# Kernel optimization log

Hardware: AMD Instinct MI355X
Metric: run time of the kernel (lower is better)

## Reference

```python
import jax, jax.numpy as jnp
import numpy as np

B, L, D_MODEL, H = 4, 2048, 1024, 16
HD = D_MODEL // H  # head_dim = 64


def _rope_tables(seq_len, dim, dtype):
    inv_freq = 1.0 / (10000.0 ** (jnp.arange(0, dim, 2, dtype=jnp.float32) / dim))
    t = jnp.arange(seq_len, dtype=jnp.float32)
    freqs = jnp.outer(t, inv_freq)  # (S, dim/2)
    return jnp.cos(freqs).astype(dtype), jnp.sin(freqs).astype(dtype)


def _apply_rope(x):
    # x: (B, H, S, d)
    cos, sin = _rope_tables(x.shape[-2], x.shape[-1], x.dtype)  # (S, d/2)
    x_even = x[..., 0::2]
    x_odd = x[..., 1::2]
    out_even = x_even * cos - x_odd * sin
    out_odd = x_even * sin + x_odd * cos
    return jnp.stack([out_even, out_odd], axis=-1).reshape(x.shape)


def setup_inputs() -> dict:
    key = jax.random.key(0)
    ks = jax.random.split(key, 9)
    s = 1.0 / np.sqrt(D_MODEL)
    inp = {
        "query": jax.random.normal(ks[0], (B, L, D_MODEL), dtype=jnp.float32),
        "Wq": jax.random.uniform(ks[1], (D_MODEL, D_MODEL), jnp.float32, -s, s),
        "bq": jax.random.uniform(ks[2], (D_MODEL,), jnp.float32, -s, s),
        "Wk": jax.random.uniform(ks[3], (D_MODEL, D_MODEL), jnp.float32, -s, s),
        "bk": jax.random.uniform(ks[4], (D_MODEL,), jnp.float32, -s, s),
        "Wv": jax.random.uniform(ks[5], (D_MODEL, D_MODEL), jnp.float32, -s, s),
        "bv": jax.random.uniform(ks[6], (D_MODEL,), jnp.float32, -s, s),
        "Wo": jax.random.uniform(ks[7], (D_MODEL, D_MODEL), jnp.float32, -s, s),
        "bo": jax.random.uniform(ks[8], (D_MODEL,), jnp.float32, -s, s),
    }
    return inp


def reference(query, Wq, bq, Wk, bk, Wv, bv, Wo, bo):
    Bq, Lq, _ = query.shape
    # projections (torch Linear: x @ W.T + b), split into heads -> (B, H, L, d)
    def proj(x, W, b):
        y = x @ W.T + b
        return y.reshape(Bq, Lq, H, HD).transpose(0, 2, 1, 3)
    q = _apply_rope(proj(query, Wq, bq))
    k = _apply_rope(proj(query, Wk, bk))
    v = proj(query, Wv, bv)
    scores = jnp.einsum("bhqd,bhkd->bhqk", q, k) / np.sqrt(HD)
    causal_mask = jnp.triu(jnp.ones((Lq, Lq), dtype=bool), k=1)
    scores = jnp.where(causal_mask[None, None, :, :], -jnp.inf, scores)
    attn = jax.nn.softmax(scores, axis=-1)
    out = jnp.einsum("bhqk,bhkd->bhqd", attn, v)
    out = out.transpose(0, 2, 1, 3).reshape(Bq, Lq, D_MODEL)
    return out @ Wo.T + bo
```

## Files before the change

kernel.cpp:

```cpp
#include <hip/hip_runtime.h>
#include <hip/hip_bf16.h>
#include <math.h>

#define L_SEQ  2048
#define DMODEL 1024
#define NHEAD  16
#define HEADD  64

typedef __attribute__((ext_vector_type(8))) short short8;
typedef __attribute__((ext_vector_type(4))) short short4v;
typedef __attribute__((ext_vector_type(4))) float f32x4;

static __device__ __forceinline__ unsigned short f2bf(float f) {
    unsigned int u = __float_as_uint(f);
    unsigned int r = (u + 0x7fffu + ((u >> 16) & 1u)) >> 16;
    return (unsigned short)r;
}

static __device__ __forceinline__ void dma16(const unsigned short* g, unsigned short* l) {
    __builtin_amdgcn_global_load_lds((const __attribute__((address_space(1))) void*)g,
                                     (__attribute__((address_space(3))) void*)l, 16, 0, 0);
}

__global__ __launch_bounds__(256) void prep(
    const float* __restrict__ query,
    const float* __restrict__ Wq, const float* __restrict__ Wk,
    const float* __restrict__ Wv, const float* __restrict__ Wo,
    unsigned short* __restrict__ xb, unsigned short* __restrict__ wdst,
    float* __restrict__ rope)
{
    int gid = blockIdx.x * 256 + threadIdx.x;
    if (gid < 2097152) {
        float4 v = reinterpret_cast<const float4*>(query)[gid];
        ushort4 o;
        o.x = f2bf(v.x); o.y = f2bf(v.y); o.z = f2bf(v.z); o.w = f2bf(v.w);
        reinterpret_cast<ushort4*>(xb)[gid] = o;
    } else if (gid < 2097152 + 1048576) {
        int i = gid - 2097152;
        int which = i >> 18;
        const float* src = which == 0 ? Wq : which == 1 ? Wk : which == 2 ? Wv : Wo;
        float4 v = reinterpret_cast<const float4*>(src)[i & 262143];
        ushort4 o;
        o.x = f2bf(v.x); o.y = f2bf(v.y); o.z = f2bf(v.z); o.w = f2bf(v.w);
        reinterpret_cast<ushort4*>(wdst)[i] = o;
    } else if (gid < 2097152 + 1048576 + 65536) {
        int i = gid - (2097152 + 1048576);
        int lpos = i >> 5, i2 = i & 31;
        float inv_f = expf(-0.28782313662425574f * (float)i2);
        float ang = (float)lpos * inv_f;
        rope[2 * i]     = cosf(ang);
        rope[2 * i + 1] = sinf(ang);
    }
}

#define BKP 32

__global__ __launch_bounds__(256) void proj_qkv(
    const unsigned short* __restrict__ X,
    const unsigned short* __restrict__ Wqkv,
    const float* __restrict__ bq_,
    const float* __restrict__ bk_,
    const float* __restrict__ bv_,
    const float* __restrict__ rope,
    unsigned short* __restrict__ Qb,
    unsigned short* __restrict__ Kb,
    unsigned short* __restrict__ Vr)
{
    __shared__ unsigned short pool[24576];
    unsigned short* a_ring = pool;
    unsigned short* b_ring = pool + 12288;

    const int tid  = threadIdx.x;
    const int lane = tid & 63;
    const int w    = tid >> 6;
    const int wm   = w & 1, wn = w >> 1;
    const int quad = lane >> 4, l16 = lane & 15;

    const int orig = blockIdx.y * 24 + blockIdx.x;
    const int xcd  = orig & 7;
    const int k    = orig >> 3;
    const int by   = xcd * 8 + (k & 7);
    const int bx   = k >> 3;
    const int m0   = by * 128;
    const int n0   = bx * 128;

    const int sel = bx >> 3;
    const float* bias   = sel == 0 ? bq_ : (sel == 1 ? bk_ : bv_);
    unsigned short* out = sel == 0 ? Qb  : (sel == 1 ? Kb  : Vr);

    const int st_row = lane >> 2;
    const int st_col = (((lane & 3) ^ ((lane >> 3) & 3)) << 3);
    const int rd = ((quad ^ ((l16 >> 1) & 3)) << 3);

    f32x4 acc[4][4];
#pragma unroll
    for (int i = 0; i < 4; ++i)
#pragma unroll
        for (int j = 0; j < 4; ++j) acc[i][j] = (f32x4){0.f, 0.f, 0.f, 0.f};

    const unsigned short* Xs = X    + (size_t)(m0 + w * 32 + st_row) * DMODEL + st_col;
    const unsigned short* Ws = Wqkv + (size_t)(n0 + w * 32 + st_row) * DMODEL + st_col;
    const int ldsA0 = (w * 32) * BKP, ldsA1 = (w * 32 + 16) * BKP;

#pragma unroll
    for (int p = 0; p < 2; ++p) {
        const int kk = p * BKP;
        dma16(Xs + kk,               a_ring + p * 4096 + ldsA0);
        dma16(Xs + 16 * DMODEL + kk, a_ring + p * 4096 + ldsA1);
        dma16(Ws + kk,               b_ring + p * 4096 + ldsA0);
        dma16(Ws + 16 * DMODEL + kk, b_ring + p * 4096 + ldsA1);
    }
    asm volatile("s_waitcnt vmcnt(4)" ::: "memory");
    __builtin_amdgcn_s_barrier();

    for (int kt = 0; kt < 32; ++kt) {
        const int slot = (kt % 3) * 4096;
        const int ps   = ((kt + 2) % 3) * 4096;
        const int kk   = ((kt + 2) & 31) * BKP;

        short8 af[4], bf[2];
#pragma unroll
        for (int i = 0; i < 4; ++i)
            af[i] = *reinterpret_cast<const short8*>(
                &a_ring[slot + (wm * 64 + i * 16 + l16) * BKP + rd]);
#pragma unroll
        for (int j = 0; j < 2; ++j)
            bf[j] = *reinterpret_cast<const short8*>(
                &b_ring[slot + (wn * 64 + j * 16 + l16) * BKP + rd]);
        dma16(Xs + kk,               a_ring + ps + ldsA0);
        dma16(Xs + 16 * DMODEL + kk, a_ring + ps + ldsA1);
        __builtin_amdgcn_s_barrier();
        asm volatile("s_waitcnt lgkmcnt(0)" ::: "memory");
        __builtin_amdgcn_sched_barrier(0);
        __builtin_amdgcn_s_setprio(1);
#pragma unroll
        for (int i = 0; i < 4; ++i)
#pragma unroll
            for (int j = 0; j < 2; ++j)
                acc[i][j] = __builtin_amdgcn_mfma_f32_16x16x32_bf16(af[i], bf[j], acc[i][j], 0, 0, 0);
        __builtin_amdgcn_s_setprio(0);
        __builtin_amdgcn_s_barrier();

#pragma unroll
        for (int j = 0; j < 2; ++j)
            bf[j] = *reinterpret_cast<const short8*>(
                &b_ring[slot + (wn * 64 + (2 + j) * 16 + l16) * BKP + rd]);
        dma16(Ws + kk,               b_ring + ps + ldsA0);
        dma16(Ws + 16 * DMODEL + kk, b_ring + ps + ldsA1);
        __builtin_amdgcn_s_barrier();
        asm volatile("s_waitcnt lgkmcnt(0)" ::: "memory");
        __builtin_amdgcn_sched_barrier(0);
        __builtin_amdgcn_s_setprio(1);
#pragma unroll
        for (int i = 0; i < 4; ++i)
#pragma unroll
            for (int j = 0; j < 2; ++j)
                acc[i][2 + j] = __builtin_amdgcn_mfma_f32_16x16x32_bf16(af[i], bf[j], acc[i][2 + j], 0, 0, 0);
        __builtin_amdgcn_s_setprio(0);
        asm volatile("s_waitcnt vmcnt(4)" ::: "memory");
        __builtin_amdgcn_s_barrier();
    }
    asm volatile("s_waitcnt vmcnt(0)" ::: "memory");
    __builtin_amdgcn_s_barrier();

#pragma unroll
    for (int jf = 0; jf < 4; ++jf) {
        int nl = wn * 64 + jf * 16 + l16;
        int nn = (bx & 7) * 128 + nl;
        float bval = bias[nn];
        int d  = nn & (HEADD - 1);
        float sgn = (d & 1) ? 1.0f : -1.0f;
        int i2 = d >> 1;
#pragma unroll
        for (int mf = 0; mf < 4; ++mf) {
#pragma unroll
            for (int r = 0; r < 4; ++r) {
                int ml = wm * 64 + mf * 16 + quad * 4 + r;
                int lpos = (m0 + ml) & (L_SEQ - 1);
                float v = acc[mf][jf][r] + bval;
                if (sel < 2) {
                    float p = __shfl_xor(v, 1);
                    float2 cs = *reinterpret_cast<const float2*>(&rope[(size_t)(lpos * 32 + i2) * 2]);
                    v = v * cs.x + sgn * cs.y * p;
                    if (sel == 0) v *= 0.18033688011112042f;
                }
                pool[(sel < 2) ? (ml * 136 + nl) : (nl * 136 + ml)] = f2bf(v);
            }
        }
    }
    __builtin_amdgcn_s_barrier();

    const int b     = m0 >> 11;
    const int lpos0 = m0 & (L_SEQ - 1);
#pragma unroll
    for (int i = 0; i < 8; ++i) {
        int g   = i * 256 + tid;
        int row = g >> 4;
        int c8  = (g & 15) * 8;
        int4 val = *reinterpret_cast<const int4*>(&pool[row * 136 + c8]);
        size_t addr;
        if (sel < 2) {
            int n_g = (bx & 7) * 128 + c8;
            int h = n_g >> 6, d = n_g & 63;
            addr = ((size_t)(b * NHEAD + h) * L_SEQ + (lpos0 + row)) * HEADD + d;
        } else {
            int n_g = (bx & 7) * 128 + row;
            int h = n_g >> 6, d = n_g & 63;
            addr = ((size_t)(b * NHEAD + h) * HEADD + d) * L_SEQ + lpos0 + c8;
        }
        *reinterpret_cast<int4*>(out + addr) = val;
    }
}

__global__ __launch_bounds__(256) void attn_fwd(
    const unsigned short* __restrict__ Q,
    const unsigned short* __restrict__ K,
    const unsigned short* __restrict__ Vt,
    unsigned short* __restrict__ Oa)
{
    __shared__ unsigned short k_lds[2][64 * 64];
    __shared__ unsigned short v_lds[2][64 * 64];
    const int tid  = threadIdx.x;
    const int lane = tid & 63;
    const int w    = tid >> 6;
    const int quad = lane >> 4, l16 = lane & 15;
    const int pair = blockIdx.y;
    const int bh   = blockIdx.x;
    const size_t base = (size_t)bh * L_SEQ * HEADD;
    const int b = bh >> 4, h = bh & 15;

    const int srow  = lane >> 3;
    const int sslot = lane & 7;
    const int ssw   = ((sslot ^ srow) << 3);
    const unsigned short* Ksrc = K  + base + (size_t)(w * 8 + srow) * HEADD + ssw;
    const unsigned short* Vsrc = Vt + base + (size_t)(w * 8 + srow) * L_SEQ + ssw;
    const int d0 = (w * 8) * 64;
    const int d1 = (32 + w * 8) * 64;
    const int swr = (l16 & 7);

    for (int half = 0; half < 2; ++half) {
        const int s = half ? (15 - pair) : pair;
        const int qrow0 = s * 128 + w * 16 + l16;
        const int qrow1 = qrow0 + 64;
        const int kbmax = 2 * s + 1;

        short8 qf0[2], qf1[2];
#pragma unroll
        for (int ks = 0; ks < 2; ++ks) {
            qf0[ks] = *reinterpret_cast<const short8*>(Q + base + (size_t)qrow0 * HEADD + ks * 32 + quad * 8);
            qf1[ks] = *reinterpret_cast<const short8*>(Q + base + (size_t)qrow1 * HEADD + ks * 32 + quad * 8);
        }

        f32x4 o0[4], o1[4];
#pragma unroll
        for (int nt = 0; nt < 4; ++nt) {
            o0[nt] = (f32x4){0.f, 0.f, 0.f, 0.f};
            o1[nt] = (f32x4){0.f, 0.f, 0.f, 0.f};
        }
        float lsum0 = 0.f, lsum1 = 0.f;

        dma16(Ksrc,                 &k_lds[0][d0]);
        dma16(Ksrc + 32 * HEADD,    &k_lds[0][d1]);
        dma16(Vsrc,                 &v_lds[0][d0]);
        dma16(Vsrc + 32 * L_SEQ,    &v_lds[0][d1]);
        asm volatile("s_waitcnt vmcnt(0)" ::: "memory");
        __builtin_amdgcn_s_barrier();

        int cur = 0;
        for (int kb = 0; kb <= kbmax; ++kb) {
            const int kn = (kb + 1) <= kbmax ? (kb + 1) : 0;
            const int nb = cur ^ 1;
            dma16(Ksrc + (size_t)(kn * 64) * HEADD,        &k_lds[nb][d0]);
            dma16(Ksrc + (size_t)(kn * 64 + 32) * HEADD,   &k_lds[nb][d1]);
            dma16(Vsrc + kn * 64,                          &v_lds[nb][d0]);
            dma16(Vsrc + kn * 64 + 32 * L_SEQ,             &v_lds[nb][d1]);

            f32x4 st0[4], st1[4];
#pragma unroll
            for (int nt = 0; nt < 4; ++nt) {
                st0[nt] = (f32x4){0.f, 0.f, 0.f, 0.f};
                st1[nt] = (f32x4){0.f, 0.f, 0.f, 0.f};
            }
            __builtin_amdgcn_s_setprio(1);
#pragma unroll
            for (int ks = 0; ks < 2; ++ks)
#pragma unroll
                for (int nt = 0; nt < 4; ++nt) {
                    short8 kf = *reinterpret_cast<const short8*>(
                        &k_lds[cur][(nt * 16 + l16) * 64 + (((ks * 4 + quad) ^ swr) << 3)]);
                    st0[nt] = __builtin_amdgcn_mfma_f32_16x16x32_bf16(kf, qf0[ks], st0[nt], 0, 0, 0);
                    st1[nt] = __builtin_amdgcn_mfma_f32_16x16x32_bf16(kf, qf1[ks], st1[nt], 0, 0, 0);
                }
            __builtin_amdgcn_s_setprio(0);

            if (kb >= 2 * s) {
#pragma unroll
                for (int nt = 0; nt < 4; ++nt)
#pragma unroll
                    for (int r = 0; r < 4; ++r) {
                        int seqcol = kb * 64 + nt * 16 + quad * 4 + r;
                        if (seqcol > qrow0) st0[nt][r] = -INFINITY;
                    }
            }
            if (kb == kbmax) {
#pragma unroll
                for (int nt = 0; nt < 4; ++nt)
#pragma unroll
                    for (int r = 0; r < 4; ++r) {
                        int seqcol = kb * 64 + nt * 16 + quad * 4 + r;
                        if (seqcol > qrow1) st1[nt][r] = -INFINITY;
                    }
            }

            short4v pfrag0[4], pfrag1[4];
#pragma unroll
            for (int nt = 0; nt < 4; ++nt) {
                float p0 = __builtin_amdgcn_exp2f(st0[nt][0]);
                float p1 = __builtin_amdgcn_exp2f(st0[nt][1]);
                float p2 = __builtin_amdgcn_exp2f(st0[nt][2]);
                float p3 = __builtin_amdgcn_exp2f(st0[nt][3]);
                lsum0 += (p0 + p1) + (p2 + p3);
                unsigned u0 = __float_as_uint(p0) + 0x8000u;
                unsigned u1 = __float_as_uint(p1) + 0x8000u;
                unsigned u2 = __float_as_uint(p2) + 0x8000u;
                unsigned u3 = __float_as_uint(p3) + 0x8000u;
                union { unsigned u[2]; short4v v; } pk;
                pk.u[0] = (u0 >> 16) | (u1 & 0xffff0000u);
                pk.u[1] = (u2 >> 16) | (u3 & 0xffff0000u);
                pfrag0[nt] = pk.v;

                float q0e = __builtin_amdgcn_exp2f(st1[nt][0]);
                float q1e = __builtin_amdgcn_exp2f(st1[nt][1]);
                float q2e = __builtin_amdgcn_exp2f(st1[nt][2]);
                float q3e = __builtin_amdgcn_exp2f(st1[nt][3]);
                lsum1 += (q0e + q1e) + (q2e + q3e);
                unsigned v0 = __float_as_uint(q0e) + 0x8000u;
                unsigned v1 = __float_as_uint(q1e) + 0x8000u;
                unsigned v2 = __float_as_uint(q2e) + 0x8000u;
                unsigned v3 = __float_as_uint(q3e) + 0x8000u;
                union { unsigned u[2]; short4v v; } pk1;
                pk1.u[0] = (v0 >> 16) | (v1 & 0xffff0000u);
                pk1.u[1] = (v2 >> 16) | (v3 & 0xffff0000u);
                pfrag1[nt] = pk1.v;
            }

            __builtin_amdgcn_s_setprio(1);
#pragma unroll
            for (int c = 0; c < 4; ++c)
#pragma unroll
                for (int nt2 = 0; nt2 < 4; ++nt2) {
                    short4v vf = *reinterpret_cast<const short4v*>(
                        &v_lds[cur][(nt2 * 16 + l16) * 64 +
                                    (((c * 2 + (quad >> 1)) ^ swr) << 3) + ((quad & 1) << 2)]);
                    o0[nt2] = __builtin_amdgcn_mfma_f32_16x16x16bf16_1k(pfrag0[c], vf, o0[nt2], 0, 0, 0);
                    o1[nt2] = __builtin_amdgcn_mfma_f32_16x16x16bf16_1k(pfrag1[c], vf, o1[nt2], 0, 0, 0);
                }
            __builtin_amdgcn_s_setprio(0);

            asm volatile("s_waitcnt vmcnt(0)" ::: "memory");
            __builtin_amdgcn_s_barrier();
            cur ^= 1;
        }

        lsum0 += __shfl_xor(lsum0, 16);
        lsum0 += __shfl_xor(lsum0, 32);
        lsum1 += __shfl_xor(lsum1, 16);
        lsum1 += __shfl_xor(lsum1, 32);
        float rs0[4], rs1[4];
#pragma unroll
        for (int r = 0; r < 4; ++r) {
            rs0[r] = __shfl(lsum0, quad * 4 + r);
            rs1[r] = __shfl(lsum1, quad * 4 + r);
        }
#pragma unroll
        for (int r = 0; r < 4; ++r) {
            float inv0 = 1.0f / rs0[r];
            float inv1 = 1.0f / rs1[r];
            int lg0 = s * 128 + w * 16 + quad * 4 + r;
            int lg1 = lg0 + 64;
#pragma unroll
            for (int nt = 0; nt < 4; ++nt) {
                int d = nt * 16 + l16;
                Oa[(size_t)(b * L_SEQ + lg0) * DMODEL + h * HEADD + d] = f2bf(o0[nt][r] * inv0);
                Oa[(size_t)(b * L_SEQ + lg1) * DMODEL + h * HEADD + d] = f2bf(o1[nt][r] * inv1);
            }
        }
    }
}

__global__ __launch_bounds__(256) void out_gemm(
    const unsigned short* __restrict__ X,
    const unsigned short* __restrict__ W,
    const float* __restrict__ bias,
    float* __restrict__ out)
{
    __shared__ unsigned short a_lds[3][128 * BKP];
    __shared__ unsigned short b_lds[3][128 * BKP];
    const int tid  = threadIdx.x;
    const int lane = tid & 63;
    const int w    = tid >> 6;
    const int wm   = w & 1, wn = w >> 1;
    const int quad = lane >> 4, l16 = lane & 15;

    const int orig = blockIdx.y * 8 + blockIdx.x;
    const int xcd  = orig & 7;
    const int k    = orig >> 3;
    const int m0   = (xcd * 8 + (k & 7)) * 128;
    const int n0   = (k >> 3) * 128;

    const int st_row = lane >> 2;
    const int st_col = (((lane & 3) ^ ((lane >> 3) & 3)) << 3);
    const int rd = ((quad ^ ((l16 >> 1) & 3)) << 3);

    f32x4 acc[4][4];
#pragma unroll
    for (int i = 0; i < 4; ++i)
#pragma unroll
        for (int j = 0; j < 4; ++j) acc[i][j] = (f32x4){0.f, 0.f, 0.f, 0.f};

    const unsigned short* Xs = X + (size_t)(m0 + w * 32 + st_row) * DMODEL + st_col;
    const unsigned short* Ws = W + (size_t)(n0 + w * 32 + st_row) * DMODEL + st_col;
    const int ldsA0 = (w * 32) * BKP, ldsA1 = (w * 32 + 16) * BKP;

#pragma unroll
    for (int p = 0; p < 2; ++p) {
        const int kk = p * BKP;
        dma16(Xs + kk,               &a_lds[p][ldsA0]);
        dma16(Xs + 16 * DMODEL + kk, &a_lds[p][ldsA1]);
        dma16(Ws + kk,               &b_lds[p][ldsA0]);
        dma16(Ws + 16 * DMODEL + kk, &b_lds[p][ldsA1]);
    }
    asm volatile("s_waitcnt vmcnt(4)" ::: "memory");
    __builtin_amdgcn_s_barrier();

    for (int kt = 0; kt < 32; ++kt) {
        const int slot = kt % 3;
        const int ps   = (kt + 2) % 3;
        const int kk   = ((kt + 2) & 31) * BKP;

        dma16(Xs + kk,               &a_lds[ps][ldsA0]);
        dma16(Xs + 16 * DMODEL + kk, &a_lds[ps][ldsA1]);
        dma16(Ws + kk,               &b_lds[ps][ldsA0]);
        dma16(Ws + 16 * DMODEL + kk, &b_lds[ps][ldsA1]);

        short8 af[4], bf[4];
#pragma unroll
        for (int i = 0; i < 4; ++i)
            af[i] = *reinterpret_cast<const short8*>(
                &a_lds[slot][(wm * 64 + i * 16 + l16) * BKP + rd]);
#pragma unroll
        for (int j = 0; j < 4; ++j)
            bf[j] = *reinterpret_cast<const short8*>(
                &b_lds[slot][(wn * 64 + j * 16 + l16) * BKP + rd]);
        asm volatile("s_waitcnt lgkmcnt(0)" ::: "memory");
        __builtin_amdgcn_sched_barrier(0);
        __builtin_amdgcn_s_setprio(1);
#pragma unroll
        for (int i = 0; i < 4; ++i)
#pragma unroll
            for (int j = 0; j < 4; ++j)
                acc[i][j] = __builtin_amdgcn_mfma_f32_16x16x32_bf16(af[i], bf[j], acc[i][j], 0, 0, 0);
        __builtin_amdgcn_s_setprio(0);
        asm volatile("s_waitcnt vmcnt(4)" ::: "memory");
        __builtin_amdgcn_s_barrier();
    }
    asm volatile("s_waitcnt vmcnt(0)" ::: "memory");

#pragma unroll
    for (int nt = 0; nt < 4; ++nt) {
        int n_g = n0 + wn * 64 + nt * 16 + l16;
        float bv = bias[n_g];
#pragma unroll
        for (int mt = 0; mt < 4; ++mt)
#pragma unroll
            for (int r = 0; r < 4; ++r) {
                int m_g = m0 + wm * 64 + mt * 16 + quad * 4 + r;
                out[(size_t)m_g * DMODEL + n_g] = acc[mt][nt][r] + bv;
            }
    }
}

extern "C" void kernel_launch(void* const* d_in, const int* in_sizes, int n_in,
                              void* d_out, int out_size, void* d_ws, size_t ws_size,
                              hipStream_t stream) {
    const float* query = (const float*)d_in[0];
    const float* Wq = (const float*)d_in[1];
    const float* bq = (const float*)d_in[2];
    const float* Wk = (const float*)d_in[3];
    const float* bk = (const float*)d_in[4];
    const float* Wv = (const float*)d_in[5];
    const float* bv = (const float*)d_in[6];
    const float* Wo = (const float*)d_in[7];
    const float* bo = (const float*)d_in[8];
    float* out = (float*)d_out;

    unsigned short* ws  = (unsigned short*)d_ws;
    unsigned short* xb  = ws;
    unsigned short* wqb = xb  + (size_t)8388608;
    unsigned short* wkb = wqb + 1048576;
    unsigned short* wvb = wkb + 1048576;
    unsigned short* wob = wvb + 1048576;
    unsigned short* Qb  = wob + 1048576;
    unsigned short* Kb  = Qb  + 8388608;
    unsigned short* Vr  = Kb  + 8388608;
    unsigned short* Ab  = Vr  + 8388608;
    float* rope = (float*)(Ab + 8388608);

    (void)wkb; (void)wvb;

    prep<<<12545, 256, 0, stream>>>(query, Wq, Wk, Wv, Wo, xb, wqb, rope);

    proj_qkv<<<dim3(24, 64), 256, 0, stream>>>(xb, wqb, bq, bk, bv, rope, Qb, Kb, Vr);
    attn_fwd<<<dim3(64, 8), 256, 0, stream>>>(Qb, Kb, Vr, Ab);
    out_gemm<<<dim3(8, 64), 256, 0, stream>>>(Ab, wob, bo, out);
}
```

Baseline: 272.0 us.

## Widen QKV projection tile to 128x256 with 512-thread blocks

The QKV projection kernel now uses 512-thread blocks that each compute a 128x256 output tile instead of 128x128, halving the grid and the number of times each X tile is loaded. The inner loop merges the two half-N MFMA phases into a single phase with one barrier pair per k-step, and the epilogue is staged in two 128-column passes through the shared pool. This aims to cut redundant global loads and barrier overhead, at the cost of higher LDS use per block, more registers per wave, and fewer blocks to spread across CUs.

```diff
diff --git a/kernel.cpp b/kernel.cpp
--- a/kernel.cpp
+++ b/kernel.cpp
@@ -55,7 +55,7 @@
 
 #define BKP 32
 
-__global__ __launch_bounds__(256) void proj_qkv(
+__global__ __launch_bounds__(512, 4) void proj_qkv(
     const unsigned short* __restrict__ X,
     const unsigned short* __restrict__ Wqkv,
     const float* __restrict__ bq_,
@@ -66,7 +66,7 @@
     unsigned short* __restrict__ Kb,
     unsigned short* __restrict__ Vr)
 {
-    __shared__ unsigned short pool[24576];
+    __shared__ unsigned short pool[36864];
     unsigned short* a_ring = pool;
     unsigned short* b_ring = pool + 12288;
 
@@ -76,15 +76,15 @@
     const int wm   = w & 1, wn = w >> 1;
     const int quad = lane >> 4, l16 = lane & 15;
 
-    const int orig = blockIdx.y * 24 + blockIdx.x;
+    const int orig = blockIdx.y * 12 + blockIdx.x;
     const int xcd  = orig & 7;
     const int k    = orig >> 3;
     const int by   = xcd * 8 + (k & 7);
-    const int bx   = k >> 3;
+    const int bxp  = k >> 3;
     const int m0   = by * 128;
-    const int n0   = bx * 128;
-
-    const int sel = bx >> 3;
+    const int n0   = bxp * 256;
+
+    const int sel = bxp >> 2;
     const float* bias   = sel == 0 ? bq_ : (sel == 1 ? bk_ : bv_);
     unsigned short* out = sel == 0 ? Qb  : (sel == 1 ? Kb  : Vr);
 
@@ -98,37 +98,40 @@
 #pragma unroll
         for (int j = 0; j < 4; ++j) acc[i][j] = (f32x4){0.f, 0.f, 0.f, 0.f};
 
-    const unsigned short* Xs = X    + (size_t)(m0 + w * 32 + st_row) * DMODEL + st_col;
+    const unsigned short* Xs = X    + (size_t)(m0 + w * 16 + st_row) * DMODEL + st_col;
     const unsigned short* Ws = Wqkv + (size_t)(n0 + w * 32 + st_row) * DMODEL + st_col;
-    const int ldsA0 = (w * 32) * BKP, ldsA1 = (w * 32 + 16) * BKP;
+    const int ldsA  = (w * 16) * BKP;
+    const int ldsB0 = (w * 32) * BKP, ldsB1 = (w * 32 + 16) * BKP;
 
 #pragma unroll
     for (int p = 0; p < 2; ++p) {
         const int kk = p * BKP;
-        dma16(Xs + kk,               a_ring + p * 4096 + ldsA0);
-        dma16(Xs + 16 * DMODEL + kk, a_ring + p * 4096 + ldsA1);
-        dma16(Ws + kk,               b_ring + p * 4096 + ldsA0);
-        dma16(Ws + 16 * DMODEL + kk, b_ring + p * 4096 + ldsA1);
-    }
-    asm volatile("s_waitcnt vmcnt(4)" ::: "memory");
+        dma16(Xs + kk,               a_ring + p * 4096 + ldsA);
+        dma16(Ws + kk,               b_ring + p * 8192 + ldsB0);
+        dma16(Ws + 16 * DMODEL + kk, b_ring + p * 8192 + ldsB1);
+    }
+    asm volatile("s_waitcnt vmcnt(3)" ::: "memory");
     __builtin_amdgcn_s_barrier();
 
     for (int kt = 0; kt < 32; ++kt) {
-        const int slot = (kt % 3) * 4096;
-        const int ps   = ((kt + 2) % 3) * 4096;
-        const int kk   = ((kt + 2) & 31) * BKP;
-
-        short8 af[4], bf[2];
+        const int sA = (kt % 3) * 4096;
+        const int sB = (kt % 3) * 8192;
+        const int pA = ((kt + 2) % 3) * 4096;
+        const int pB = ((kt + 2) % 3) * 8192;
+        const int kk = ((kt + 2) & 31) * BKP;
+
+        short8 af[4], bf[4];
 #pragma unroll
         for (int i = 0; i < 4; ++i)
             af[i] = *reinterpret_cast<const short8*>(
-                &a_ring[slot + (wm * 64 + i * 16 + l16) * BKP + rd]);
-#pragma unroll
-        for (int j = 0; j < 2; ++j)
+                &a_ring[sA + (wm * 64 + i * 16 + l16) * BKP + rd]);
+#pragma unroll
+        for (int j = 0; j < 4; ++j)
             bf[j] = *reinterpret_cast<const short8*>(
-                &b_ring[slot + (wn * 64 + j * 16 + l16) * BKP + rd]);
-        dma16(Xs + kk,               a_ring + ps + ldsA0);
-        dma16(Xs + 16 * DMODEL + kk, a_ring + ps + ldsA1);
+                &b_ring[sB + (wn * 64 + j * 16 + l16) * BKP + rd]);
+        dma16(Xs + kk,               a_ring + pA + ldsA);
+        dma16(Ws + kk,               b_ring + pB + ldsB0);
+        dma16(Ws + 16 * DMODEL + kk, b_ring + pB + ldsB1);
         __builtin_amdgcn_s_barrier();
         asm volatile("s_waitcnt lgkmcnt(0)" ::: "memory");
         __builtin_amdgcn_sched_barrier(0);
@@ -136,79 +139,68 @@
 #pragma unroll
         for (int i = 0; i < 4; ++i)
 #pragma unroll
-            for (int j = 0; j < 2; ++j)
+            for (int j = 0; j < 4; ++j)
                 acc[i][j] = __builtin_amdgcn_mfma_f32_16x16x32_bf16(af[i], bf[j], acc[i][j], 0, 0, 0);
         __builtin_amdgcn_s_setprio(0);
-        __builtin_amdgcn_s_barrier();
-
-#pragma unroll
-        for (int j = 0; j < 2; ++j)
-            bf[j] = *reinterpret_cast<const short8*>(
-                &b_ring[slot + (wn * 64 + (2 + j) * 16 + l16) * BKP + rd]);
-        dma16(Ws + kk,               b_ring + ps + ldsA0);
-        dma16(Ws + 16 * DMODEL + kk, b_ring + ps + ldsA1);
-        __builtin_amdgcn_s_barrier();
-        asm volatile("s_waitcnt lgkmcnt(0)" ::: "memory");
-        __builtin_amdgcn_sched_barrier(0);
-        __builtin_amdgcn_s_setprio(1);
-#pragma unroll
-        for (int i = 0; i < 4; ++i)
-#pragma unroll
-            for (int j = 0; j < 2; ++j)
-                acc[i][2 + j] = __builtin_amdgcn_mfma_f32_16x16x32_bf16(af[i], bf[j], acc[i][2 + j], 0, 0, 0);
-        __builtin_amdgcn_s_setprio(0);
-        asm volatile("s_waitcnt vmcnt(4)" ::: "memory");
+        asm volatile("s_waitcnt vmcnt(3)" ::: "memory");
         __builtin_amdgcn_s_barrier();
     }
     asm volatile("s_waitcnt vmcnt(0)" ::: "memory");
     __builtin_amdgcn_s_barrier();
 
-#pragma unroll
-    for (int jf = 0; jf < 4; ++jf) {
-        int nl = wn * 64 + jf * 16 + l16;
-        int nn = (bx & 7) * 128 + nl;
-        float bval = bias[nn];
-        int d  = nn & (HEADD - 1);
-        float sgn = (d & 1) ? 1.0f : -1.0f;
-        int i2 = d >> 1;
-#pragma unroll
-        for (int mf = 0; mf < 4; ++mf) {
-#pragma unroll
-            for (int r = 0; r < 4; ++r) {
-                int ml = wm * 64 + mf * 16 + quad * 4 + r;
-                int lpos = (m0 + ml) & (L_SEQ - 1);
-                float v = acc[mf][jf][r] + bval;
-                if (sel < 2) {
-                    float p = __shfl_xor(v, 1);
-                    float2 cs = *reinterpret_cast<const float2*>(&rope[(size_t)(lpos * 32 + i2) * 2]);
-                    v = v * cs.x + sgn * cs.y * p;
-                    if (sel == 0) v *= 0.18033688011112042f;
-                }
-                pool[(sel < 2) ? (ml * 136 + nl) : (nl * 136 + ml)] = f2bf(v);
-            }
-        }
-    }
-    __builtin_amdgcn_s_barrier();
-
     const int b     = m0 >> 11;
     const int lpos0 = m0 & (L_SEQ - 1);
 #pragma unroll
-    for (int i = 0; i < 8; ++i) {
-        int g   = i * 256 + tid;
-        int row = g >> 4;
-        int c8  = (g & 15) * 8;
-        int4 val = *reinterpret_cast<const int4*>(&pool[row * 136 + c8]);
-        size_t addr;
-        if (sel < 2) {
-            int n_g = (bx & 7) * 128 + c8;
-            int h = n_g >> 6, d = n_g & 63;
-            addr = ((size_t)(b * NHEAD + h) * L_SEQ + (lpos0 + row)) * HEADD + d;
-        } else {
-            int n_g = (bx & 7) * 128 + row;
-            int h = n_g >> 6, d = n_g & 63;
-            addr = ((size_t)(b * NHEAD + h) * HEADD + d) * L_SEQ + lpos0 + c8;
-        }
-        *reinterpret_cast<int4*>(out + addr) = val;
+    for (int t = 0; t < 2; ++t) {
+        if ((wn >> 1) == t) {
+#pragma unroll
+            for (int jf = 0; jf < 4; ++jf) {
+                int nl = (wn & 1) * 64 + jf * 16 + l16;
+                int nn = (bxp & 3) * 256 + t * 128 + nl;
+                float bval = bias[nn];
+                int d  = nn & (HEADD - 1);
+                float sgn = (d & 1) ? 1.0f : -1.0f;
+                int i2 = d >> 1;
+#pragma unroll
+                for (int mf = 0; mf < 4; ++mf) {
+#pragma unroll
+                    for (int r = 0; r < 4; ++r) {
+                        int ml = wm * 64 + mf * 16 + quad * 4 + r;
+                        int lpos = (m0 + ml) & (L_SEQ - 1);
+                        float v = acc[mf][jf][r] + bval;
+                        if (sel < 2) {
+                            float p = __shfl_xor(v, 1);
+                            float2 cs = *reinterpret_cast<const float2*>(&rope[(size_t)(lpos * 32 + i2) * 2]);
+                            v = v * cs.x + sgn * cs.y * p;
+                            if (sel == 0) v *= 0.18033688011112042f;
+                        }
+                        pool[(sel < 2) ? (ml * 136 + nl) : (nl * 136 + ml)] = f2bf(v);
+                    }
+                }
+            }
+        }
+        asm volatile("s_waitcnt lgkmcnt(0)" ::: "memory");
+        __builtin_amdgcn_s_barrier();
+#pragma unroll
+        for (int i = 0; i < 4; ++i) {
+            int g   = i * 512 + tid;
+            int row = g >> 4;
+            int c8  = (g & 15) * 8;
+            int4 val = *reinterpret_cast<const int4*>(&pool[row * 136 + c8]);
+            size_t addr;
+            if (sel < 2) {
+                int n_g = (bxp & 3) * 256 + t * 128 + c8;
+                int h = n_g >> 6, d = n_g & 63;
+                addr = ((size_t)(b * NHEAD + h) * L_SEQ + (lpos0 + row)) * HEADD + d;
+            } else {
+                int n_g = (bxp & 3) * 256 + t * 128 + row;
+                int h = n_g >> 6, d = n_g & 63;
+                addr = ((size_t)(b * NHEAD + h) * HEADD + d) * L_SEQ + lpos0 + c8;
+            }
+            *reinterpret_cast<int4*>(out + addr) = val;
+        }
+        asm volatile("s_waitcnt lgkmcnt(0)" ::: "memory");
+        __builtin_amdgcn_s_barrier();
     }
 }
 
@@ -510,7 +502,7 @@
 
     prep<<<12545, 256, 0, stream>>>(query, Wq, Wk, Wv, Wo, xb, wqb, rope);
 
-    proj_qkv<<<dim3(24, 64), 256, 0, stream>>>(xb, wqb, bq, bk, bv, rope, Qb, Kb, Vr);
+    proj_qkv<<<dim3(12, 64), 512, 0, stream>>>(xb, wqb, bq, bk, bv, rope, Qb, Kb, Vr);
     attn_fwd<<<dim3(64, 8), 256, 0, stream>>>(Qb, Kb, Vr, Ab);
     out_gemm<<<dim3(8, 64), 256, 0, stream>>>(Ab, wob, bo, out);
 }
```

Result: slower. 277.6 us (+2.1%).
